# Performance work log

Hardware: AMD Instinct MI355X
Metric: run time of the kernel (lower is better)

## Reference

```python
import jax, jax.numpy as jnp
import numpy as np

EMBED_DIM = 1024
NUM_HEADS = 16
HEAD_DIM = EMBED_DIM // NUM_HEADS


def setup_inputs() -> dict:
    key = jax.random.key(0)
    ks = jax.random.split(key, 11)
    B, S, D = 2, 2048, EMBED_DIM
    s = 1.0 / np.sqrt(D)
    inp = {
        "query": jax.random.normal(ks[0], (B, S, D), jnp.float32),
        "key": jax.random.normal(ks[1], (B, S, D), jnp.float32),
        "value": jax.random.normal(ks[2], (B, S, D), jnp.float32),
        # torch Linear weights: [out, in]
        "Wq": jax.random.normal(ks[3], (D, D), jnp.float32) * s,
        "bq": jnp.zeros((D,), jnp.float32),
        "Wk": jax.random.normal(ks[4], (D, D), jnp.float32) * s,
        "bk": jnp.zeros((D,), jnp.float32),
        "Wv": jax.random.normal(ks[5], (D, D), jnp.float32) * s,
        "bv": jnp.zeros((D,), jnp.float32),
        "Wo": jax.random.normal(ks[6], (D, D), jnp.float32) * s,
        "bo": jnp.zeros((D,), jnp.float32),
    }
    return inp


def reference(query, key, value, Wq, bq, Wk, bk, Wv, bv, Wo, bo):
    B, Q, D = query.shape
    K = key.shape[1]
    H, Hd = NUM_HEADS, HEAD_DIM
    # NOTE: source divides by scaling = head_dim**-0.5, i.e. multiplies by sqrt(head_dim)
    scaling = float(Hd) ** (-0.5)

    q = (query @ Wq.T + bq).reshape(B, Q, H, Hd).transpose(0, 2, 1, 3)  # [B,H,Q,Hd]
    k = (key @ Wk.T + bk).reshape(B, K, H, Hd).transpose(0, 2, 1, 3)    # [B,H,K,Hd]
    v = (value @ Wv.T + bv).reshape(B, K, H, Hd).transpose(0, 2, 1, 3)  # [B,H,K,Hd]

    scores = jnp.einsum("bhqd,bhkd->bhqk", q, k) / scaling
    attn = jax.nn.softmax(scores, axis=-1)  # dropout=0 (eval)
    out = jnp.einsum("bhqk,bhkd->bhqd", attn, v)
    out = out.transpose(0, 2, 1, 3).reshape(B, Q, D)
    return out @ Wo.T + bo
```

## Files before the change

kernel.cpp:

```cpp
#include <hip/hip_runtime.h>
#include <type_traits>
#include <utility>

#define B_ 2
#define S_ 2048
#define D_ 1024
#define H_ 16
#define HD_ 64
#define KDIM 1024

typedef __attribute__((ext_vector_type(8))) short    s16x8;
typedef __attribute__((ext_vector_type(8))) _Float16 h16x8;
typedef __attribute__((ext_vector_type(4))) float    f32x4;
typedef __attribute__((ext_vector_type(4))) int      i32x4;
typedef __attribute__((ext_vector_type(2))) int      i32x2;

template <typename T, typename = void> struct mfma_takes : std::false_type {};
template <typename T>
struct mfma_takes<T, std::void_t<decltype(__builtin_amdgcn_mfma_f32_16x16x32_f16(
    std::declval<T>(), std::declval<T>(), std::declval<f32x4>(), 0, 0, 0))>>
    : std::true_type {};
using frag8 = std::conditional_t<mfma_takes<h16x8>::value, h16x8, s16x8>;

__device__ __forceinline__ f32x4 mfma_f16(frag8 a, frag8 b, f32x4 c) {
  return __builtin_amdgcn_mfma_f32_16x16x32_f16(a, b, c, 0, 0, 0);
}

__device__ __forceinline__ short f2h(float f) {
  _Float16 h = (_Float16)f;
  short s; __builtin_memcpy(&s, &h, 2);
  return s;
}
__device__ __forceinline__ int pk2h(float a, float b) {
  auto p = __builtin_amdgcn_cvt_pkrtz(a, b);
  int r; __builtin_memcpy(&r, &p, 4); return r;
}
__device__ __forceinline__ frag8 ld_frag(const short* p) {
  return __builtin_bit_cast(frag8, *(const i32x4*)p);
}
__device__ __forceinline__ float fast_exp2(float x) {
  return __builtin_amdgcn_exp2f(x);
}

typedef __attribute__((address_space(1))) const void gvoid;
typedef __attribute__((address_space(3))) void lvoid;
__device__ __forceinline__ void async_copy16(const void* g, void* l) {
  __builtin_amdgcn_global_load_lds((gvoid*)g, (lvoid*)l, 16, 0, 0);
}

#define RAW_BARRIER() asm volatile("s_barrier" ::: "memory")
#define WAITCNT_VM(n) asm volatile("s_waitcnt vmcnt(" #n ")" ::: "memory")

__global__ __launch_bounds__(256)
void conv_all(const float* __restrict__ q, const float* __restrict__ k,
              const float* __restrict__ v, const float* __restrict__ Wq,
              const float* __restrict__ Wk, const float* __restrict__ Wv,
              const float* __restrict__ Wo,
              short* __restrict__ qh, short* __restrict__ kh,
              short* __restrict__ vh, short* __restrict__ wq,
              short* __restrict__ wk, short* __restrict__ wv,
              short* __restrict__ wo) {
  const int blk = blockIdx.x;
  const float* src; short* dst; int base;
  if (blk < 2048)      { src = q;  dst = qh; base = blk; }
  else if (blk < 4096) { src = k;  dst = kh; base = blk - 2048; }
  else if (blk < 6144) { src = v;  dst = vh; base = blk - 4096; }
  else if (blk < 6656) { src = Wq; dst = wq; base = blk - 6144; }
  else if (blk < 7168) { src = Wk; dst = wk; base = blk - 6656; }
  else if (blk < 7680) { src = Wv; dst = wv; base = blk - 7168; }
  else                 { src = Wo; dst = wo; base = blk - 7680; }
  const int i = base * 2048 + threadIdx.x * 8;
  float4 a0 = *(const float4*)(src + i);
  float4 a1 = *(const float4*)(src + i + 4);
  short h[8] = { f2h(a0.x), f2h(a0.y), f2h(a0.z), f2h(a0.w),
                 f2h(a1.x), f2h(a1.y), f2h(a1.z), f2h(a1.w) };
  i32x4 ph; __builtin_memcpy(&ph, h, 16);
  *(i32x4*)(dst + i) = ph;
}

__global__ __launch_bounds__(256, 3)
void gemm_qkv(const short* __restrict__ qh, const short* __restrict__ kh,
              const short* __restrict__ vh, const short* __restrict__ wq,
              const short* __restrict__ wk, const short* __restrict__ wv,
              const float* __restrict__ bq, const float* __restrict__ bk,
              const float* __restrict__ bv, short* __restrict__ Qf,
              short* __restrict__ Kf, short* __restrict__ Vt, float QS) {
  __shared__ short As[3 * 4096];
  __shared__ short Bs[3 * 4096];

  const int blk = blockIdx.x;
  const int xcd = blk & 7, i = blk >> 3;
  const int p = (i >> 3) * 8 + xcd;
  const int bn = i & 7;
  const int z = p >> 5, bm = p & 31;
  const short* Ap = z == 0 ? qh : z == 1 ? kh : vh;
  const short* Wp = z == 0 ? wq : z == 1 ? wk : wv;
  const float* bias = z == 0 ? bq : z == 1 ? bk : bv;
  short* Out = z == 0 ? Qf : z == 1 ? Kf : Vt;
  const float scale = z == 0 ? QS : 1.0f;
  const int omode = z == 2 ? 2 : 1;

  const int t = threadIdx.x, wave = t >> 6, lane = t & 63;
  const int laneN = lane & 15, quad = lane >> 4;
  const int wm = wave & 1, wn = wave >> 1;

  f32x4 acc[4][4];
#pragma unroll
  for (int i2 = 0; i2 < 4; ++i2)
#pragma unroll
    for (int j = 0; j < 4; ++j)
#pragma unroll
      for (int r = 0; r < 4; ++r) acc[i2][j][r] = 0.f;

  auto stage = [&](int buf, int kk) {
#pragma unroll
    for (int j = 0; j < 2; ++j) {
      const int chunk = j * 256 + t;
      const int row = chunk >> 2;
      const int gg = (chunk & 3) ^ ((row >> 1) & 3);
      async_copy16(Ap + (size_t)(bm * 128 + row) * KDIM + kk + gg * 8,
                   As + buf * 4096 + chunk * 8);
      async_copy16(Wp + (size_t)(bn * 128 + row) * KDIM + kk + gg * 8,
                   Bs + buf * 4096 + chunk * 8);
    }
  };

  stage(0, 0);
  stage(1, 32);
  int buf = 0;
  for (int kk = 0; kk < KDIM; kk += 32) {
    if (kk + 64 < KDIM) {
      int nb = buf + 2; if (nb >= 3) nb -= 3;
      stage(nb, kk + 64);
      WAITCNT_VM(8);
    } else if (kk + 32 < KDIM) {
      WAITCNT_VM(4);
    } else {
      WAITCNT_VM(0);
    }
    RAW_BARRIER();

    frag8 aF[4], bF[4];
#pragma unroll
    for (int mi = 0; mi < 4; ++mi) {
      const int row = wm * 64 + mi * 16 + laneN;
      aF[mi] = ld_frag(As + buf * 4096 + row * 32 +
                       ((quad ^ ((row >> 1) & 3)) * 8));
    }
#pragma unroll
    for (int ni = 0; ni < 4; ++ni) {
      const int row = wn * 64 + ni * 16 + laneN;
      bF[ni] = ld_frag(Bs + buf * 4096 + row * 32 +
                       ((quad ^ ((row >> 1) & 3)) * 8));
    }
#pragma unroll
    for (int mi = 0; mi < 4; ++mi)
#pragma unroll
      for (int ni = 0; ni < 4; ++ni)
        acc[mi][ni] = mfma_f16(aF[mi], bF[ni], acc[mi][ni]);
    RAW_BARRIER();
    buf = buf + 1 == 3 ? 0 : buf + 1;
  }

#pragma unroll
  for (int mi = 0; mi < 4; ++mi)
#pragma unroll
    for (int ni = 0; ni < 4; ++ni) {
      const int colg = bn * 128 + wn * 64 + ni * 16 + laneN;
      const float bb = bias[colg];
      if (omode == 2) {
        const int rowg0 = bm * 128 + wm * 64 + mi * 16 + quad * 4;
        const int b = rowg0 >> 11, s0 = rowg0 & 2047;
        const int h = colg >> 6, hd = colg & 63;
        short pk[4];
#pragma unroll
        for (int r = 0; r < 4; ++r) pk[r] = f2h(acc[mi][ni][r] + bb);
        i32x2 w; __builtin_memcpy(&w, pk, 8);
        *(i32x2*)(Vt + (((size_t)(b * H_ + h)) * HD_ + hd) * S_ + s0) = w;
      } else {
#pragma unroll
        for (int r = 0; r < 4; ++r) {
          const int rowg = bm * 128 + wm * 64 + mi * 16 + quad * 4 + r;
          const int b = rowg >> 11, s = rowg & 2047;
          const int h = colg >> 6, hd = colg & 63;
          Out[(((size_t)(b * H_ + h)) * S_ + s) * HD_ + hd] =
              f2h((acc[mi][ni][r] + bb) * scale);
        }
      }
    }
}

__global__ __launch_bounds__(256, 3)
void gemm_out(const short* __restrict__ Ap, const short* __restrict__ Wp,
              const float* __restrict__ bias, float* __restrict__ Out) {
  __shared__ short As[3 * 4096];
  __shared__ short Bs[3 * 2048];
  const int blk = blockIdx.x;
  const int xcd = blk & 7, i = blk >> 3;
  const int bm = (i >> 4) * 8 + xcd;
  const int bn = i & 15;

  const int t = threadIdx.x, wave = t >> 6, lane = t & 63;
  const int laneN = lane & 15, quad = lane >> 4;
  const int wm = wave & 1, wn = wave >> 1;

  f32x4 acc[4][2];
#pragma unroll
  for (int i2 = 0; i2 < 4; ++i2)
#pragma unroll
    for (int j = 0; j < 2; ++j)
#pragma unroll
      for (int r = 0; r < 4; ++r) acc[i2][j][r] = 0.f;

  auto stage = [&](int buf, int kk) {
#pragma unroll
    for (int j = 0; j < 2; ++j) {
      const int chunk = j * 256 + t;
      const int row = chunk >> 2;
      const int gg = (chunk & 3) ^ ((row >> 1) & 3);
      async_copy16(Ap + (size_t)(bm * 128 + row) * KDIM + kk + gg * 8,
                   As + buf * 4096 + chunk * 8);
    }
    {
      const int chunk = t;
      const int row = chunk >> 2;
      const int gg = (chunk & 3) ^ ((row >> 1) & 3);
      async_copy16(Wp + (size_t)(bn * 64 + row) * KDIM + kk + gg * 8,
                   Bs + buf * 2048 + chunk * 8);
    }
  };

  stage(0, 0);
  stage(1, 32);
  int buf = 0;
  for (int kk = 0; kk < KDIM; kk += 32) {
    if (kk + 64 < KDIM) {
      int nb = buf + 2; if (nb >= 3) nb -= 3;
      stage(nb, kk + 64);
      WAITCNT_VM(6);
    } else if (kk + 32 < KDIM) {
      WAITCNT_VM(3);
    } else {
      WAITCNT_VM(0);
    }
    RAW_BARRIER();

    frag8 aF[4], bF[2];
#pragma unroll
    for (int mi = 0; mi < 4; ++mi) {
      const int row = wm * 64 + mi * 16 + laneN;
      aF[mi] = ld_frag(As + buf * 4096 + row * 32 +
                       ((quad ^ ((row >> 1) & 3)) * 8));
    }
#pragma unroll
    for (int ni = 0; ni < 2; ++ni) {
      const int row = wn * 32 + ni * 16 + laneN;
      bF[ni] = ld_frag(Bs + buf * 2048 + row * 32 +
                       ((quad ^ ((row >> 1) & 3)) * 8));
    }
#pragma unroll
    for (int mi = 0; mi < 4; ++mi)
#pragma unroll
      for (int ni = 0; ni < 2; ++ni)
        acc[mi][ni] = mfma_f16(aF[mi], bF[ni], acc[mi][ni]);
    RAW_BARRIER();
    buf = buf + 1 == 3 ? 0 : buf + 1;
  }

#pragma unroll
  for (int mi = 0; mi < 4; ++mi)
#pragma unroll
    for (int ni = 0; ni < 2; ++ni) {
      const int colg = bn * 64 + wn * 32 + ni * 16 + laneN;
      const float bb = bias[colg];
#pragma unroll
      for (int r = 0; r < 4; ++r) {
        const int rowg = bm * 128 + wm * 64 + mi * 16 + quad * 4 + r;
        Out[(size_t)rowg * 1024 + colg] = acc[mi][ni][r] + bb;
      }
    }
}

__global__ __launch_bounds__(512, 4)
void attn(const short* __restrict__ Qf, const short* __restrict__ Kf,
          const short* __restrict__ Vt_, short* __restrict__ Ow) {
  __shared__ short Ks[2 * 4096];
  __shared__ short Vts[2 * 4096];
  __shared__ short Ps[8][16 * 64];

  const int blk = blockIdx.x;
  const int xcd = blk & 7, local = blk >> 3;
  const int pair = xcd * 4 + (local >> 4);
  const int h = pair & 15, b = pair >> 4, qt = local & 15;
  const size_t head = ((size_t)b * H_ + h) * (size_t)S_ * HD_;

  const int t = threadIdx.x;
  const int wave = t >> 6, lane = t & 63;
  const int laneN = lane & 15, quad = lane >> 4;

  frag8 qf[2];
  {
    const size_t row = (size_t)qt * 128 + wave * 16 + laneN;
#pragma unroll
    for (int half = 0; half < 2; ++half)
      qf[half] = ld_frag(Qf + head + row * HD_ + half * 32 + quad * 8);
  }

  f32x4 o[4];
  float m_r = -1e30f, l_r = 0.f;
#pragma unroll
  for (int i = 0; i < 4; ++i)
#pragma unroll
    for (int j = 0; j < 4; ++j) o[i][j] = 0.f;

  const int srow = t >> 3, sg = (t & 7) ^ (srow & 7);
  const short* kp = Kf + head + (size_t)srow * HD_ + sg * 8;
  const short* vp = Vt_ + head + (size_t)srow * S_ + sg * 8;
  const int d = t * 8;

  int off[4][2];
#pragma unroll
  for (int nt = 0; nt < 4; ++nt) {
    const int row = nt * 16 + laneN;
    off[nt][0] = row * 64 + ((quad ^ (row & 7)) * 8);
    off[nt][1] = row * 64 + (((quad + 4) ^ (row & 7)) * 8);
  }

  short* const pwr = &Ps[wave][0] + laneN * 64;
  short* pw[4];
#pragma unroll
  for (int nt = 0; nt < 4; ++nt) {
    const int g = nt * 2 + (quad >> 1);
    pw[nt] = pwr + ((g + laneN) & 7) * 8 + (quad & 1) * 4;
  }
  const short* prd0 = pwr + ((quad + laneN) & 7) * 8;
  const short* prd1 = pwr + (((quad + 4) + laneN) & 7) * 8;

  async_copy16(kp, Ks + d);
  async_copy16(vp, Vts + d);
  kp += 4096; vp += 64;

#define ATTN_TILE(RBUF, DO_STAGE)                                            \
  {                                                                          \
    if (DO_STAGE) {                                                          \
      async_copy16(kp, (RBUF ? Ks : Ks + 4096) + d);                         \
      async_copy16(vp, (RBUF ? Vts : Vts + 4096) + d);                       \
      kp += 4096; vp += 64;                                                  \
      WAITCNT_VM(2);                                                         \
    } else {                                                                 \
      WAITCNT_VM(0);                                                         \
    }                                                                        \
    RAW_BARRIER();                                                           \
    const short* KbS = Ks + (RBUF ? 4096 : 0);                               \
    const short* VbS = Vts + (RBUF ? 4096 : 0);                              \
                        \
    frag8 vf[4][2];                                                          \
    _Pragma("unroll")                                                        \
    for (int dt = 0; dt < 4; ++dt) {                                         \
      vf[dt][0] = ld_frag(VbS + off[dt][0]);                                 \
      vf[dt][1] = ld_frag(VbS + off[dt][1]);                                 \
    }                                                                        \
          \
    f32x4 s[4];                                                              \
    _Pragma("unroll")                                                        \
    for (int nt = 0; nt < 4; ++nt) {                                         \
      frag8 k0 = ld_frag(KbS + off[nt][0]);                                  \
      frag8 k1 = ld_frag(KbS + off[nt][1]);                                  \
      f32x4 acc = {0.f, 0.f, 0.f, 0.f};                                      \
      acc = mfma_f16(k0, qf[0], acc);                                        \
      acc = mfma_f16(k1, qf[1], acc);                                        \
      s[nt] = acc;                                                           \
    }                                                                        \
          \
    {                                                                        \
      float mt[4];                                                           \
      _Pragma("unroll")                                                      \
      for (int nt = 0; nt < 4; ++nt)                                         \
        mt[nt] = fmaxf(fmaxf(s[nt][0], s[nt][1]),                            \
                       fmaxf(s[nt][2], s[nt][3]));                           \
      float mx = fmaxf(fmaxf(mt[0], mt[1]), fmaxf(mt[2], mt[3]));            \
      mx = fmaxf(mx, __shfl_xor(mx, 16));                                    \
      mx = fmaxf(mx, __shfl_xor(mx, 32));                                    \
      if (__any(mx > m_r + 8.f)) {         \
        const float mn = fmaxf(m_r, mx);                                     \
        const float al = fast_exp2(m_r - mn);                                \
        m_r = mn;                                                            \
        l_r *= al;                                                           \
        _Pragma("unroll")                                                    \
        for (int dt = 0; dt < 4; ++dt)                                       \
          _Pragma("unroll")                                                  \
          for (int r = 0; r < 4; ++r) o[dt][r] *= al;                        \
      }                                                                      \
      float rt[4];                                                           \
      _Pragma("unroll")                                                      \
      for (int nt = 0; nt < 4; ++nt) {                                       \
        const float p0 = fast_exp2(s[nt][0] - m_r);                          \
        const float p1 = fast_exp2(s[nt][1] - m_r);                          \
        const float p2 = fast_exp2(s[nt][2] - m_r);                          \
        const float p3 = fast_exp2(s[nt][3] - m_r);                          \
        s[nt][0] = p0; s[nt][1] = p1; s[nt][2] = p2; s[nt][3] = p3;          \
        rt[nt] = (p0 + p1) + (p2 + p3);                                      \
      }                                                                      \
      float rs = (rt[0] + rt[1]) + (rt[2] + rt[3]);                          \
      rs += __shfl_xor(rs, 16);                                              \
      rs += __shfl_xor(rs, 32);                                              \
      l_r += rs;                                                             \
    }                                                                        \
            \
    _Pragma("unroll")                                                        \
    for (int nt = 0; nt < 4; ++nt) {                                         \
      i32x2 w;                                                               \
      w[0] = pk2h(s[nt][0], s[nt][1]);                                       \
      w[1] = pk2h(s[nt][2], s[nt][3]);                                       \
      *(i32x2*)pw[nt] = w;                                                   \
    }                                                                        \
          \
    const frag8 p0 = ld_frag(prd0);                                          \
    const frag8 p1 = ld_frag(prd1);                                          \
    _Pragma("unroll")                                                        \
    for (int dt = 0; dt < 4; ++dt) {                                         \
      o[dt] = mfma_f16(vf[dt][0], p0, o[dt]);                                \
      o[dt] = mfma_f16(vf[dt][1], p1, o[dt]);                                \
    }                                                                        \
    RAW_BARRIER();                                                           \
  }

  for (int it = 0; it < 15; ++it) {
    ATTN_TILE(0, 1)
    ATTN_TILE(1, 1)
  }
  ATTN_TILE(0, 1)
  ATTN_TILE(1, 0)
#undef ATTN_TILE

  {
    const float inv = 1.0f / l_r;
    const int sgq = qt * 128 + wave * 16 + laneN;
    short* dst = Ow + ((size_t)b * S_ + sgq) * D_ + h * HD_;
#pragma unroll
    for (int dt = 0; dt < 4; ++dt) {
      short pk[4] = { f2h(o[dt][0] * inv), f2h(o[dt][1] * inv),
                      f2h(o[dt][2] * inv), f2h(o[dt][3] * inv) };
      i32x2 w; __builtin_memcpy(&w, pk, 8);
      *(i32x2*)(dst + dt * 16 + quad * 4) = w;
    }
  }
}

extern "C" void kernel_launch(void* const* d_in, const int* in_sizes, int n_in,
                              void* d_out, int out_size, void* d_ws, size_t ws_size,
                              hipStream_t stream) {
  const float* q  = (const float*)d_in[0];
  const float* k  = (const float*)d_in[1];
  const float* v  = (const float*)d_in[2];
  const float* Wq = (const float*)d_in[3];
  const float* bq = (const float*)d_in[4];
  const float* Wk = (const float*)d_in[5];
  const float* bk = (const float*)d_in[6];
  const float* Wv = (const float*)d_in[7];
  const float* bv = (const float*)d_in[8];
  const float* Wo = (const float*)d_in[9];
  const float* bo = (const float*)d_in[10];

  const size_t NTOK = (size_t)B_ * S_ * D_;
  const size_t NW   = (size_t)D_ * D_;
  short* p = (short*)d_ws;
  short* qh = p; p += NTOK;  short* kh = p; p += NTOK;  short* vh = p; p += NTOK;
  short* wq = p; p += NW;    short* wk = p; p += NW;
  short* wv = p; p += NW;    short* wo = p; p += NW;
  short* Qf = p; p += NTOK;  short* Kf = p; p += NTOK;
  short* Vt = p; p += NTOK;  short* Ow = p; p += NTOK;

  dim3 blk(256);

  conv_all<<<8192, blk, 0, stream>>>(q, k, v, Wq, Wk, Wv, Wo,
                                     qh, kh, vh, wq, wk, wv, wo);

  const float QS = 11.541560327111707f;
  gemm_qkv<<<768, blk, 0, stream>>>(qh, kh, vh, wq, wk, wv, bq, bk, bv,
                                    Qf, Kf, Vt, QS);

  attn<<<512, dim3(512), 0, stream>>>(Qf, Kf, Vt, Ow);

  gemm_out<<<512, blk, 0, stream>>>(Ow, wo, bo, (float*)d_out);
}
```

Measured before the change: 225.4 us.

## Stage GEMM epilogues through LDS and deepen attention K/V pipeline to four buffers

```diff
diff --git a/kernel.cpp b/kernel.cpp
--- a/kernel.cpp
+++ b/kernel.cpp
@@ -162,32 +162,51 @@
     buf = buf + 1 == 3 ? 0 : buf + 1;
   }
 
-#pragma unroll
-  for (int mi = 0; mi < 4; ++mi)
+  short* scr = As + wave * 1152;
+  const int h = bn * 2 + wn;
+  if (omode == 2) {
+    const int bidx = bm >> 4;
+    const int sbase = (bm * 128 + wm * 64) & 2047;
 #pragma unroll
     for (int ni = 0; ni < 4; ++ni) {
-      const int colg = bn * 128 + wn * 64 + ni * 16 + laneN;
-      const float bb = bias[colg];
-      if (omode == 2) {
-        const int rowg0 = bm * 128 + wm * 64 + mi * 16 + quad * 4;
-        const int b = rowg0 >> 11, s0 = rowg0 & 2047;
-        const int h = colg >> 6, hd = colg & 63;
+      const float bb = bias[bn * 128 + wn * 64 + ni * 16 + laneN];
+#pragma unroll
+      for (int mi = 0; mi < 4; ++mi) {
         short pk[4];
 #pragma unroll
         for (int r = 0; r < 4; ++r) pk[r] = f2h(acc[mi][ni][r] + bb);
         i32x2 w; __builtin_memcpy(&w, pk, 8);
-        *(i32x2*)(Vt + (((size_t)(b * H_ + h)) * HD_ + hd) * S_ + s0) = w;
-      } else {
-#pragma unroll
-        for (int r = 0; r < 4; ++r) {
-          const int rowg = bm * 128 + wm * 64 + mi * 16 + quad * 4 + r;
-          const int b = rowg >> 11, s = rowg & 2047;
-          const int h = colg >> 6, hd = colg & 63;
-          Out[(((size_t)(b * H_ + h)) * S_ + s) * HD_ + hd] =
+        *(i32x2*)(scr + laneN * 72 + mi * 16 + quad * 4) = w;
+      }
+#pragma unroll
+      for (int j = 0; j < 2; ++j) {
+        const int ff = lane * 2 + j, hdr = ff >> 3, ch = ff & 7;
+        i32x4 v = *(const i32x4*)(scr + hdr * 72 + ch * 8);
+        *(i32x4*)(Vt + (((size_t)(bidx * H_ + h)) * HD_ + ni * 16 + hdr) * S_ +
+                  sbase + ch * 8) = v;
+      }
+    }
+  } else {
+#pragma unroll
+    for (int mi = 0; mi < 4; ++mi) {
+#pragma unroll
+      for (int ni = 0; ni < 4; ++ni) {
+        const float bb = bias[bn * 128 + wn * 64 + ni * 16 + laneN];
+#pragma unroll
+        for (int r = 0; r < 4; ++r)
+          scr[(quad * 4 + r) * 72 + ni * 16 + laneN] =
               f2h((acc[mi][ni][r] + bb) * scale);
-        }
       }
-    }
+#pragma unroll
+      for (int j = 0; j < 2; ++j) {
+        const int ff = lane * 2 + j, row = ff >> 3, ch = ff & 7;
+        const int rowg = bm * 128 + wm * 64 + mi * 16 + row;
+        const int bidx = rowg >> 11, s = rowg & 2047;
+        i32x4 v = *(const i32x4*)(scr + row * 72 + ch * 8);
+        *(i32x4*)(Out + (((size_t)(bidx * H_ + h)) * S_ + s) * HD_ + ch * 8) = v;
+      }
+    }
+  }
 }
 
 __global__ __launch_bounds__(256, 3)
@@ -267,25 +286,31 @@
     buf = buf + 1 == 3 ? 0 : buf + 1;
   }
 
-#pragma unroll
-  for (int mi = 0; mi < 4; ++mi)
+  float* scr = (float*)As + wave * 576;
+#pragma unroll
+  for (int mi = 0; mi < 4; ++mi) {
 #pragma unroll
     for (int ni = 0; ni < 2; ++ni) {
-      const int colg = bn * 64 + wn * 32 + ni * 16 + laneN;
-      const float bb = bias[colg];
-#pragma unroll
-      for (int r = 0; r < 4; ++r) {
-        const int rowg = bm * 128 + wm * 64 + mi * 16 + quad * 4 + r;
-        Out[(size_t)rowg * 1024 + colg] = acc[mi][ni][r] + bb;
-      }
-    }
+      const float bb = bias[bn * 64 + wn * 32 + ni * 16 + laneN];
+#pragma unroll
+      for (int r = 0; r < 4; ++r)
+        scr[(quad * 4 + r) * 36 + ni * 16 + laneN] = acc[mi][ni][r] + bb;
+    }
+#pragma unroll
+    for (int j = 0; j < 2; ++j) {
+      const int ff = lane * 2 + j, row = ff >> 3, ch = ff & 7;
+      const int rowg = bm * 128 + wm * 64 + mi * 16 + row;
+      f32x4 v = *(const f32x4*)(scr + row * 36 + ch * 4);
+      *(f32x4*)(Out + (size_t)rowg * 1024 + bn * 64 + wn * 32 + ch * 4) = v;
+    }
+  }
 }
 
 __global__ __launch_bounds__(512, 4)
 void attn(const short* __restrict__ Qf, const short* __restrict__ Kf,
           const short* __restrict__ Vt_, short* __restrict__ Ow) {
-  __shared__ short Ks[2 * 4096];
-  __shared__ short Vts[2 * 4096];
+  __shared__ short Ks[4 * 4096];
+  __shared__ short Vts[4 * 4096];
   __shared__ short Ps[8][16 * 64];
 
   const int blk = blockIdx.x;
@@ -336,23 +361,26 @@
   const short* prd0 = pwr + ((quad + laneN) & 7) * 8;
   const short* prd1 = pwr + (((quad + 4) + laneN) & 7) * 8;
 
-  async_copy16(kp, Ks + d);
-  async_copy16(vp, Vts + d);
+  async_copy16(kp, Ks + d);  async_copy16(vp, Vts + d);
   kp += 4096; vp += 64;
-
-#define ATTN_TILE(RBUF, DO_STAGE)                                            \
+  async_copy16(kp, Ks + 4096 + d);  async_copy16(vp, Vts + 4096 + d);
+  kp += 4096; vp += 64;
+
+#define ATTN_TILE(B0, STG)                                                   \
   {                                                                          \
-    if (DO_STAGE) {                                                          \
-      async_copy16(kp, (RBUF ? Ks : Ks + 4096) + d);                         \
-      async_copy16(vp, (RBUF ? Vts : Vts + 4096) + d);                       \
+    if (STG == 1) {                                                          \
+      async_copy16(kp, Ks + (((B0) + 2) & 3) * 4096 + d);                    \
+      async_copy16(vp, Vts + (((B0) + 2) & 3) * 4096 + d);                   \
       kp += 4096; vp += 64;                                                  \
+      WAITCNT_VM(4);                                                         \
+    } else if (STG == 2) {                                                   \
       WAITCNT_VM(2);                                                         \
     } else {                                                                 \
       WAITCNT_VM(0);                                                         \
     }                                                                        \
     RAW_BARRIER();                                                           \
-    const short* KbS = Ks + (RBUF ? 4096 : 0);                               \
-    const short* VbS = Vts + (RBUF ? 4096 : 0);                              \
+    const short* KbS = Ks + (B0) * 4096;                                     \
+    const short* VbS = Vts + (B0) * 4096;                                    \
                         \
     frag8 vf[4][2];                                                          \
     _Pragma("unroll")                                                        \
@@ -362,6 +390,7 @@
     }                                                                        \
           \
     f32x4 s[4];                                                              \
+    __builtin_amdgcn_s_setprio(1);                                           \
     _Pragma("unroll")                                                        \
     for (int nt = 0; nt < 4; ++nt) {                                         \
       frag8 k0 = ld_frag(KbS + off[nt][0]);                                  \
@@ -371,6 +400,7 @@
       acc = mfma_f16(k1, qf[1], acc);                                        \
       s[nt] = acc;                                                           \
     }                                                                        \
+    __builtin_amdgcn_s_setprio(0);                                           \
           \
     {                                                                        \
       float mt[4];                                                           \
@@ -417,20 +447,25 @@
           \
     const frag8 p0 = ld_frag(prd0);                                          \
     const frag8 p1 = ld_frag(prd1);                                          \
+    __builtin_amdgcn_s_setprio(1);                                           \
     _Pragma("unroll")                                                        \
     for (int dt = 0; dt < 4; ++dt) {                                         \
       o[dt] = mfma_f16(vf[dt][0], p0, o[dt]);                                \
       o[dt] = mfma_f16(vf[dt][1], p1, o[dt]);                                \
     }                                                                        \
-    RAW_BARRIER();                                                           \
-  }
-
-  for (int it = 0; it < 15; ++it) {
+    __builtin_amdgcn_s_setprio(0);                                           \
+  }
+
+  for (int it = 0; it < 7; ++it) {
     ATTN_TILE(0, 1)
     ATTN_TILE(1, 1)
+    ATTN_TILE(2, 1)
+    ATTN_TILE(3, 1)
   }
   ATTN_TILE(0, 1)
-  ATTN_TILE(1, 0)
+  ATTN_TILE(1, 1)
+  ATTN_TILE(2, 2)
+  ATTN_TILE(3, 0)
 #undef ATTN_TILE
 
   {
```

Measured after the change: 224.2 us. About the same (-0.5%).
